# Kernel optimization log

Measured on AMD Instinct MI355X. Metric: run time of the kernel, lower is better.

The kernel has to match this reference:

```python
import jax, jax.numpy as jnp
import numpy as np

N, C, H, W = 8, 128, 56, 56
CO = C // 8  # 16


def setup_inputs() -> dict:
    key = jax.random.key(0)
    k1, k2, k3, k4 = jax.random.split(key, 4)
    x = jax.random.normal(k1, (N, C, H, W), dtype=jnp.float32)
    # p_3: Conv2d(c*35 -> c//8, 1x1). The unfold channel order is (c, kh=5, kw=7),
    # so the 1x1 conv over c*35 channels is exactly a dilated 5x7 conv with
    # weight [CO, C, 5, 7] and rhs_dilation (2, 3).
    w3 = jax.random.normal(k2, (CO, C, 5, 7), dtype=jnp.float32) * 0.02
    w4 = jax.random.normal(k3, (CO, CO), dtype=jnp.float32) * 0.1
    w5 = jax.random.normal(k4, (C, CO), dtype=jnp.float32) * 0.1
    return {"x": x, "w3": w3, "w4": w4, "w5": w5}


def reference(x, w3, w4, w5):
    # Fused equivalent of: unfold(5x1, dil 2, pad 4) -> unfold(1x7, dil 3, pad 9)
    # -> 1x1 conv (c*35 -> c//8). Padding (4,4)/(9,9) keeps 'same' spatial size.
    y = jax.lax.conv_general_dilated(
        x, w3,
        window_strides=(1, 1),
        padding=((4, 4), (9, 9)),
        rhs_dilation=(2, 3),
        dimension_numbers=("NCHW", "OIHW", "NCHW"),
    )  # [N, CO, H, W]
    y = jnp.einsum("oc,nchw->nohw", w4, y)  # p_4: 1x1 conv CO->CO
    y = jnp.einsum("oc,nchw->nohw", w5, y)  # p_5: 1x1 conv CO->C
    return y
```

## Files before the change

### kernel.cpp

```cpp
#include <hip/hip_runtime.h>

#define BN 8
#define BC 128
#define BH 56
#define BW 56
#define HW 3136
#define NTAP 35
#define WS_WC 71680

typedef unsigned short u16;
typedef unsigned int u32;
typedef __bf16 bf16x8 __attribute__((ext_vector_type(8)));
typedef float f32x4 __attribute__((ext_vector_type(4)));

__device__ __forceinline__ u16 f2b(float f) {
    unsigned u = __float_as_uint(f);
    return (u16)((u + 0x7FFFu + ((u >> 16) & 1u)) >> 16);
}
__device__ __forceinline__ u32 pack2(float a, float b) {
    return (u32)f2b(a) | ((u32)f2b(b) << 16);
}

__global__ __launch_bounds__(256) void prep_w(
    const float* __restrict__ w3, const float* __restrict__ w4,
    const float* __restrict__ w5, u16* __restrict__ ws)
{
    int i = blockIdx.x * 256 + threadIdx.x;
    if (i < WS_WC) {
        int j = i & 7, lane = (i >> 3) & 63, r = i >> 9;
        int tap = r % NTAP, cc = r / NTAP;
        int q = lane >> 4, lm = lane & 15;
        ws[i] = f2b(w3[(lm * BC + cc * 32 + q * 8 + j) * NTAP + tap]);
    } else if (i < WS_WC + 4096) {
        int i2 = i - WS_WC;
        int j = i2 & 7, lane = (i2 >> 3) & 63, ot = i2 >> 9;
        int q = lane >> 4, lm = lane & 15, o = ot * 16 + lm, k = q * 8 + j;
        float s = 0.f;
        if (k < 16)
            for (int c = 0; c < 16; ++c) s += w5[o * 16 + c] * w4[c * 16 + k];
        ws[i] = f2b(s);
    }
}

#define COLW 40
#define XSBUF 32000
#define U32BUF 8000
#define Y3_OFF 64000
#define SMEM_SZ 69632

__global__ __launch_bounds__(512, 4) void conv_mfma(
    const float* __restrict__ x, const u16* __restrict__ wsT,
    float* __restrict__ out)
{
    __shared__ __align__(16) char smem[SMEM_SZ];
    u16* y3T = (u16*)(smem + Y3_OFF);
    float* cbuf = (float*)smem;

    const int n = blockIdx.x & 7;
    const int h = blockIdx.x >> 3;
    const int tid = threadIdx.x, lane = tid & 63, wv = tid >> 6;
    const int g = wv & 3, wp = wv >> 2;
    const int q = lane >> 4, lm = lane & 15;
    const int c0 = wp * 32 + lm;
    const int c1 = c0 + 16;
    const int t0 = 9 * g;
    const int ntap = (g == 3) ? 8 : 9;

    float4 sa[3], sb[3];
#define SLOAD(CC) do {                                                        \
        _Pragma("unroll")                                                     \
        for (int u = 0; u < 3; ++u) {                                         \
            int it = tid + u * 512;                                           \
            if (it < 1120) {                                                  \
                int r = it / 224, rem = it % 224;                             \
                int cp = rem / 14, wq = rem % 14;                             \
                int gr = h - 4 + 2 * r;                                       \
                if ((unsigned)gr < BH) {                                      \
                    const float* px = x + ((size_t)(n * BC + (CC) * 32 + 2 * cp) * BH + gr) * BW + 4 * wq; \
                    sa[u] = *(const float4*)px;                               \
                    sb[u] = *(const float4*)(px + HW);                        \
                }                                                             \
            }                                                                 \
        }                                                                     \
    } while (0)

#define SWRITE(BUF) do {                                                      \
        u32* xb = (u32*)(smem + (BUF) * XSBUF);                               \
        _Pragma("unroll")                                                     \
        for (int u = 0; u < 3; ++u) {                                         \
            int it = tid + u * 512;                                           \
            if (it < 1120) {                                                  \
                int r = it / 224, rem = it % 224;                             \
                int cp = rem / 14, wq = rem % 14;                             \
                int gr = h - 4 + 2 * r;                                       \
                if ((unsigned)gr < BH) {                                      \
                    u32* d = xb + (r * 80 + 9 + 4 * wq) * 20 + cp;            \
                    d[0]  = pack2(sa[u].x, sb[u].x);                          \
                    d[20] = pack2(sa[u].y, sb[u].y);                          \
                    d[40] = pack2(sa[u].z, sb[u].z);                          \
                    d[60] = pack2(sa[u].w, sb[u].w);                          \
                }                                                             \
            }                                                                 \
        }                                                                     \
    } while (0)

    SLOAD(0);
    for (int i = tid; i < 3840; i += 512) {
        int cp = i & 15, t = i >> 4;
        int pc = t % 24, t2 = t / 24;
        int r = t2 % 5, bb = t2 / 5;
        int col = pc < 9 ? pc : 56 + pc;
        ((u32*)smem)[bb * U32BUF + (r * 80 + col) * 20 + cp] = 0u;
    }
    int bad0 = 0, bad1 = 0, nb = 0;
    #pragma unroll
    for (int r = 0; r < 5; ++r) {
        int gr = h - 4 + 2 * r;
        if ((unsigned)gr >= BH) { if (nb == 0) bad0 = r; else bad1 = r; ++nb; }
    }
    for (int i = tid; i < nb * 1792; i += 512) {
        int cp = i & 15, t = i >> 4;
        int w = t % 56, t2 = t / 56;
        int bb = t2 & 1, r = (t2 >> 1) ? bad1 : bad0;
        ((u32*)smem)[bb * U32BUF + (r * 80 + 9 + w) * 20 + cp] = 0u;
    }
    ((u32*)(y3T + (tid >> 3) * 40))[8 + (tid & 7)] = 0u;
    SWRITE(0);
    __syncthreads();

    f32x4 acc0 = {0.f, 0.f, 0.f, 0.f};
    f32x4 acc1 = {0.f, 0.f, 0.f, 0.f};

    #pragma unroll
    for (int cc = 0; cc < 4; ++cc) {
        const int buf = cc & 1;
        bf16x8 a[9];
        #pragma unroll
        for (int tt = 0; tt < 9; ++tt) {
            if (tt < ntap)
                a[tt] = *(const bf16x8*)(wsT + (size_t)(cc * NTAP + t0 + tt) * 512 + lane * 8);
        }
        if (cc < 3) SLOAD(cc + 1);
        const u16* xsb = (const u16*)(smem + buf * XSBUF);
        #pragma unroll
        for (int tt = 0; tt < 9; ++tt) {
            if (tt < ntap) {
                const int t = t0 + tt;
                const int kh = t / 7, kw = t - 7 * kh;
                const u16* xrow = xsb + (size_t)(kh * 80 + 3 * kw) * COLW + q * 8;
                bf16x8 b0 = *(const bf16x8*)(xrow + (size_t)c0 * COLW);
                acc0 = __builtin_amdgcn_mfma_f32_16x16x32_bf16(a[tt], b0, acc0, 0, 0, 0);
                bf16x8 b1 = *(const bf16x8*)(xrow + (size_t)c1 * COLW);
                acc1 = __builtin_amdgcn_mfma_f32_16x16x32_bf16(a[tt], b1, acc1, 0, 0, 0);
            }
        }
        if (cc < 3) {
            SWRITE(buf ^ 1);
            __syncthreads();
        }
    }

    if (g > 0) {
        float* cb = cbuf + (size_t)(((wp * 3 + (g - 1)) * 2) * 64 + lane) * 4;
        *(f32x4*)cb = acc0;
        *(f32x4*)(cb + 256) = acc1;
    }
    __syncthreads();
    if (g == 0) {
        #pragma unroll
        for (int p = 0; p < 3; ++p) {
            const float* cb = cbuf + (size_t)(((wp * 3 + p) * 2) * 64 + lane) * 4;
            f32x4 v0 = *(const f32x4*)cb;
            f32x4 v1 = *(const f32x4*)(cb + 256);
            acc0[0] += v0[0]; acc0[1] += v0[1]; acc0[2] += v0[2]; acc0[3] += v0[3];
            acc1[0] += v1[0]; acc1[1] += v1[1]; acc1[2] += v1[2]; acc1[3] += v1[3];
        }
        const bool ok1 = (c1 < BW);
        *(u32*)(y3T + c0 * 40 + q * 4)     = pack2(acc0[0], acc0[1]);
        *(u32*)(y3T + c0 * 40 + q * 4 + 2) = pack2(acc0[2], acc0[3]);
        *(u32*)(y3T + c1 * 40 + q * 4)     = ok1 ? pack2(acc1[0], acc1[1]) : 0u;
        *(u32*)(y3T + c1 * 40 + q * 4 + 2) = ok1 ? pack2(acc1[2], acc1[3]) : 0u;
    }
    __syncthreads();

    const int ct = wv & 3, og = wv >> 2;
    const int wgc = ct * 16 + lm;
    bf16x8 bfrag = *(const bf16x8*)(y3T + (size_t)wgc * 40 + q * 8);
    #pragma unroll
    for (int i = 0; i < 4; ++i) {
        const int ot = 4 * og + i;
        bf16x8 afrag = *(const bf16x8*)(wsT + WS_WC + (size_t)(ot * 64 + lane) * 8);
        f32x4 c2 = {0.f, 0.f, 0.f, 0.f};
        c2 = __builtin_amdgcn_mfma_f32_16x16x32_bf16(afrag, bfrag, c2, 0, 0, 0);
        if (wgc < BW) {
            const int o = ot * 16 + q * 4;
            float* po = out + ((size_t)(n * BC + o) * BH + h) * BW + wgc;
            po[0]      = c2[0];
            po[HW]     = c2[1];
            po[2 * HW] = c2[2];
            po[3 * HW] = c2[3];
        }
    }
#undef SLOAD
#undef SWRITE
}

extern "C" void kernel_launch(void* const* d_in, const int* in_sizes, int n_in,
                              void* d_out, int out_size, void* d_ws, size_t ws_size,
                              hipStream_t stream)
{
    (void)in_sizes; (void)n_in; (void)out_size; (void)ws_size;
    const float* x  = (const float*)d_in[0];
    const float* w3 = (const float*)d_in[1];
    const float* w4 = (const float*)d_in[2];
    const float* w5 = (const float*)d_in[3];
    u16* ws = (u16*)d_ws;

    prep_w<<<296, 256, 0, stream>>>(w3, w4, w5, ws);
    conv_mfma<<<BN * BH, 512, 0, stream>>>(x, ws, (float*)d_out);
}
```

Measured before the change: 85.17 us.

## Fuse weight prep into conv kernel with a flag-based grid barrier

Removes the separate prep_w launch. Each block of the conv kernel now converts a slice of the weights to bf16 into the workspace. A software grid barrier (per-block release flags plus spinning) makes every block wait until all weights are written before the MFMA loop. This saves one kernel launch and its inter-kernel gap. In exchange it relies on all 448 blocks being co-resident, and the flags are never reset. On repeated calls the barrier therefore passes at once, so blocks may read weight slices while other blocks are still rewriting them.

```diff
diff --git a/kernel.cpp b/kernel.cpp
--- a/kernel.cpp
+++ b/kernel.cpp
@@ -7,6 +7,8 @@
 #define HW 3136
 #define NTAP 35
 #define WS_WC 71680
+#define WS_FLAGS (1u << 20)
+#define MAGIC 0x9E3779B9u
 
 typedef unsigned short u16;
 typedef unsigned int u32;
@@ -19,27 +21,6 @@
 }
 __device__ __forceinline__ u32 pack2(float a, float b) {
     return (u32)f2b(a) | ((u32)f2b(b) << 16);
-}
-
-__global__ __launch_bounds__(256) void prep_w(
-    const float* __restrict__ w3, const float* __restrict__ w4,
-    const float* __restrict__ w5, u16* __restrict__ ws)
-{
-    int i = blockIdx.x * 256 + threadIdx.x;
-    if (i < WS_WC) {
-        int j = i & 7, lane = (i >> 3) & 63, r = i >> 9;
-        int tap = r % NTAP, cc = r / NTAP;
-        int q = lane >> 4, lm = lane & 15;
-        ws[i] = f2b(w3[(lm * BC + cc * 32 + q * 8 + j) * NTAP + tap]);
-    } else if (i < WS_WC + 4096) {
-        int i2 = i - WS_WC;
-        int j = i2 & 7, lane = (i2 >> 3) & 63, ot = i2 >> 9;
-        int q = lane >> 4, lm = lane & 15, o = ot * 16 + lm, k = q * 8 + j;
-        float s = 0.f;
-        if (k < 16)
-            for (int c = 0; c < 16; ++c) s += w5[o * 16 + c] * w4[c * 16 + k];
-        ws[i] = f2b(s);
-    }
 }
 
 #define COLW 40
@@ -48,14 +29,17 @@
 #define Y3_OFF 64000
 #define SMEM_SZ 69632
 
-__global__ __launch_bounds__(512, 4) void conv_mfma(
-    const float* __restrict__ x, const u16* __restrict__ wsT,
-    float* __restrict__ out)
+__global__ __launch_bounds__(512, 4) void conv_fused(
+    const float* __restrict__ x, const float* __restrict__ w3,
+    const float* __restrict__ w4, const float* __restrict__ w5,
+    u16* __restrict__ ws, float* __restrict__ out)
 {
     __shared__ __align__(16) char smem[SMEM_SZ];
     u16* y3T = (u16*)(smem + Y3_OFF);
     float* cbuf = (float*)smem;
 
+    const u16* wsT = ws;
+    u32* flags = (u32*)(ws + WS_FLAGS);
     const int n = blockIdx.x & 7;
     const int h = blockIdx.x >> 3;
     const int tid = threadIdx.x, lane = tid & 63, wv = tid >> 6;
@@ -105,6 +89,25 @@
     } while (0)
 
     SLOAD(0);
+
+    {
+        int i = blockIdx.x * 512 + tid;
+        if (i < WS_WC) {
+            int j = i & 7, ln = (i >> 3) & 63, r = i >> 9;
+            int tap = r % NTAP, cc = r / NTAP;
+            int qq = ln >> 4, ll = ln & 15;
+            ws[i] = f2b(w3[(ll * BC + cc * 32 + qq * 8 + j) * NTAP + tap]);
+        } else if (i < WS_WC + 4096) {
+            int i2 = i - WS_WC;
+            int j = i2 & 7, ln = (i2 >> 3) & 63, ot = i2 >> 9;
+            int qq = ln >> 4, ll = ln & 15, o = ot * 16 + ll, k = qq * 8 + j;
+            float s = 0.f;
+            if (k < 16)
+                for (int c = 0; c < 16; ++c) s += w5[o * 16 + c] * w4[c * 16 + k];
+            ws[i] = f2b(s);
+        }
+    }
+
     for (int i = tid; i < 3840; i += 512) {
         int cp = i & 15, t = i >> 4;
         int pc = t % 24, t2 = t / 24;
@@ -126,7 +129,20 @@
     }
     ((u32*)(y3T + (tid >> 3) * 40))[8 + (tid & 7)] = 0u;
     SWRITE(0);
+
+    __threadfence();
     __syncthreads();
+    if (tid == 0)
+        __hip_atomic_store(&flags[blockIdx.x], MAGIC,
+                           __ATOMIC_RELEASE, __HIP_MEMORY_SCOPE_AGENT);
+    for (;;) {
+        int mine = (tid >= BN * BH) ? 1 :
+            (__hip_atomic_load(&flags[tid], __ATOMIC_RELAXED,
+                               __HIP_MEMORY_SCOPE_AGENT) == MAGIC);
+        if (__syncthreads_and(mine)) break;
+        __builtin_amdgcn_s_sleep(2);
+    }
+    __threadfence();
 
     f32x4 acc0 = {0.f, 0.f, 0.f, 0.f};
     f32x4 acc1 = {0.f, 0.f, 0.f, 0.f};
@@ -216,6 +232,5 @@
     const float* w5 = (const float*)d_in[3];
     u16* ws = (u16*)d_ws;
 
-    prep_w<<<296, 256, 0, stream>>>(w3, w4, w5, ws);
-    conv_mfma<<<BN * BH, 512, 0, stream>>>(x, ws, (float*)d_out);
-}
+    conv_fused<<<BN * BH, 512, 0, stream>>>(x, w3, w4, w5, ws, (float*)d_out);
+}
```

Result: slower. 204.0 us (+139.5%).
